# Performance work log

Hardware: AMD Instinct MI355X
Metric: run time of the kernel (lower is better)

The kernel has to match this reference:

```python
import jax, jax.numpy as jnp
import numpy as np

WIN = 32  # hardcoded window size in the original module


def _find(parent, x):
    while parent[x] != x:
        parent[x] = parent[parent[x]]
        x = parent[x]
    return x


def _label_background(bg):
    # 4-connected component labeling of True pixels; False pixels get label 0
    w = bg.shape[0]
    n = w * w
    parent = np.arange(n, dtype=np.int64)
    flat = bg.ravel()
    idx = np.arange(n).reshape(w, w)
    e1 = np.concatenate([idx[:, :-1].ravel(), idx[:-1, :].ravel()])
    e2 = np.concatenate([idx[:, 1:].ravel(), idx[1:, :].ravel()])
    for a, b in zip(e1, e2):
        if flat[a] and flat[b]:
            ra, rb = _find(parent, a), _find(parent, b)
            if ra != rb:
                parent[ra] = rb
    labels = np.zeros(n, dtype=np.int64)
    root2lab = {}
    nxt = 1
    for i in range(n):
        if flat[i]:
            r = _find(parent, i)
            if r not in root2lab:
                root2lab[r] = nxt
                nxt += 1
            labels[i] = root2lab[r]
    return labels


def _malis(seg, e1, e2, costs, pos):
    # Kruskal-style maximin MALIS edge weighting (descending affinity order).
    # Pairs involving segment label 0 (foreground / non-background) are excluded.
    n = seg.shape[0]
    parent = np.arange(n, dtype=np.int64)
    cnts = [({int(seg[i]): 1} if seg[i] != 0 else {}) for i in range(n)]
    w = np.zeros(costs.shape[0], dtype=np.int64)
    order = np.argsort(-costs, kind='stable')
    for e in order:
        a, b = _find(parent, e1[e]), _find(parent, e2[e])
        if a == b:
            continue
        ca, cb = cnts[a], cnts[b]
        if len(ca) > len(cb):  # small-to-large merge
            a, b, ca, cb = b, a, cb, ca
        common = 0
        for l, c in ca.items():
            if l in cb:
                common += c * cb[l]
        if pos:
            w[e] = common
        else:
            sa = sum(ca.values())
            sb = sum(cb.values())
            w[e] = sa * sb - common
        for l, c in ca.items():
            cb[l] = cb.get(l, 0) + c
        parent[a] = b
        cnts[a] = {}
    return w


def _malis_weights_full(pred, target):
    pred = np.asarray(pred)
    target = np.asarray(target)
    B, C, H, W = pred.shape
    weights_n = np.zeros(pred.shape, dtype=np.float32)
    weights_p = np.zeros(pred.shape, dtype=np.float32)
    idx = np.arange(WIN * WIN).reshape(WIN, WIN)
    e1 = np.concatenate([idx[:, :-1].ravel(), idx[:-1, :].ravel()])
    e2 = np.concatenate([idx[:, 1:].ravel(), idx[1:, :].ravel()])
    for r in range(H // WIN):
        for c in range(W // WIN):
            p = pred[:, :, r * WIN:(r + 1) * WIN, c * WIN:(c + 1) * WIN]
            t = target[:, :, r * WIN:(r + 1) * WIN, c * WIN:(c + 1) * WIN]
            costs_h = (p[:, :, :, :-1] + p[:, :, :, 1:]).reshape(B, -1)
            costs_v = (p[:, :, :-1, :] + p[:, :, 1:, :]).reshape(B, -1)
            costs = np.concatenate([costs_h, costs_v], 1)
            gt_h = (t[:, :, :, :-1] + t[:, :, :, 1:]).reshape(B, -1)
            gt_v = (t[:, :, :-1, :] + t[:, :, 1:, :]).reshape(B, -1)
            gt = np.concatenate([gt_h, gt_v], 1)
            costs_n = costs.copy()
            costs_p = costs.copy()
            costs_n[gt > 20] = 20
            costs_p[gt < 10] = 0
            gt = np.minimum(gt, 20)
            for i in range(B):
                seg = _label_background(t[i, 0] == 0)
                wn = _malis(seg, e1, e2, costs_n[i].astype(np.float32), 0).astype(np.float64)
                wp = _malis(seg, e1, e2, costs_p[i].astype(np.float32), 1).astype(np.float64)
                if wn.sum() > 0:
                    wn = wn / wn.sum()
                if wp.sum() > 0:
                    wp = wp / wp.sum()
                wn[gt[i] >= 10] = 0
                wp[gt[i] < 20] = 0
                half = WIN * (WIN - 1)
                for wsrc, wdst in ((wn, weights_n), (wp, weights_p)):
                    wh = wsrc[:half].reshape(WIN, WIN - 1)
                    wv = wsrc[half:].reshape(WIN - 1, WIN)
                    nw = np.zeros((WIN, WIN), dtype=np.float64)
                    nw[:, :-1] += wh
                    nw[:, 1:] += wh
                    nw[:-1, :] += wv
                    nw[1:, :] += wv
                    wdst[i, 0, r * WIN:(r + 1) * WIN, c * WIN:(c + 1) * WIN] = nw
    return weights_n, weights_p


def setup_inputs() -> dict:
    key = jax.random.key(0)
    k1, k2 = jax.random.split(key)
    y_true = jax.random.randint(k1, (4, 1, 256, 256), 0, 2).astype(jnp.float32) * 20.0
    y_pred = jax.random.uniform(k2, (4, 1, 256, 256), dtype=jnp.float32) * 20.0
    return {"y_true": y_true, "y_pred": y_pred}


def reference(y_true, y_pred):
    malis_lr = 1.0
    malis_lr_pos = 1.0
    out_sd = (jax.ShapeDtypeStruct(y_pred.shape, jnp.float32),
              jax.ShapeDtypeStruct(y_pred.shape, jnp.float32))
    weights_n, weights_p = jax.pure_callback(
        _malis_weights_full, out_sd,
        jax.lax.stop_gradient(y_pred), jax.lax.stop_gradient(y_true))
    loss_n = y_pred ** 2
    loss_p = (20.0 - y_pred) ** 2
    return (malis_lr * loss_n * weights_n + malis_lr_pos * loss_p * weights_p).sum()
```

## Files before the change

kernel.cpp:

```cpp
#include <hip/hip_runtime.h>

#define NPIX   1024
#define NEH    992
#define NEDGE  1984
#define SORTN  2048
#define CHUNK  8
#define NMERGE 1023
#define NIL    0xFFFFu

__device__ __forceinline__ void edge_ab(int e, int& a, int& b) {
    if (e < NEH) { int y = e / 31; int x = e - y * 31; a = y * 32 + x; b = a + 1; }
    else         { int ev = e - NEH; a = ev; b = ev + 32; }
}

__device__ __forceinline__ uint4 add4(uint4 x, uint4 y) {
    return make_uint4(x.x + y.x, x.y + y.y, x.z + y.z, x.w + y.w);
}
__device__ __forceinline__ uint4 sub4(uint4 x, uint4 y) {
    return make_uint4(x.x - y.x, x.y - y.y, x.z - y.z, x.w - y.w);
}

__device__ __forceinline__ unsigned rdl32(unsigned v, int lane) {
    return (unsigned)__builtin_amdgcn_readlane((int)v, lane);
}
__device__ __forceinline__ unsigned long long rdl64(unsigned long long v, int lane) {
    unsigned lo = (unsigned)__builtin_amdgcn_readlane((int)(unsigned)v, lane);
    unsigned hi = (unsigned)__builtin_amdgcn_readlane((int)(unsigned)(v >> 32), lane);
    return ((unsigned long long)hi << 32) | lo;
}

__device__ void ccl_body(char* smem, int* kprimeSh,
                         const float* __restrict__ t_glob,
                         unsigned short* __restrict__ pixLab_g,
                         int* __restrict__ Kg, int tileId) {
    const int tid = threadIdx.x;
    const int bat = tileId >> 6;
    const int tile = tileId & 63;
    const int tr = tile >> 3, tc = tile & 7;

    unsigned short* labS = (unsigned short*)smem;
    unsigned int*   cntS = (unsigned int*)(smem + 2048);
    unsigned char*  bgS  = (unsigned char*)(smem + 20480);

    for (int i = tid; i < NPIX; i += 256) {
        int y = i >> 5, x = i & 31;
        int gidx = bat * 65536 + (tr * 32 + y) * 256 + (tc * 32 + x);
        bgS[i] = (t_glob[gidx] == 0.0f) ? 1 : 0;
    }
    __syncthreads();

    if (tid < 64) {
        const int lane = tid;
        if (lane < 32) {
            #pragma unroll
            for (int x = 0; x < 32; x++) {
                int i = lane * 32 + x;
                labS[i] = bgS[i] ? (unsigned short)i : (unsigned short)NIL;
            }
        }
        while (true) {
            bool changed = false;
            if (lane < 32) {
                const int base = lane * 32;
                unsigned short v[32];
                #pragma unroll
                for (int x = 0; x < 32; x++) v[x] = labS[base + x];
                unsigned run = NIL;
                #pragma unroll
                for (int x = 0; x < 32; x++) {
                    unsigned val = v[x];
                    if (val == NIL) { run = NIL; }
                    else { unsigned nv = min(run, val); changed |= (nv != val); v[x] = (unsigned short)nv; run = nv; }
                }
                run = NIL;
                #pragma unroll
                for (int x = 31; x >= 0; x--) {
                    unsigned val = v[x];
                    if (val == NIL) { run = NIL; }
                    else { unsigned nv = min(run, val); changed |= (nv != val); v[x] = (unsigned short)nv; run = nv; }
                }
                #pragma unroll
                for (int x = 0; x < 32; x++) labS[base + x] = v[x];
            }
            if (lane < 32) {
                unsigned short c[32];
                #pragma unroll
                for (int k = 0; k < 32; k++) c[k] = labS[k * 32 + lane];
                unsigned run = NIL;
                #pragma unroll
                for (int k = 0; k < 32; k++) {
                    unsigned val = c[k];
                    if (val == NIL) { run = NIL; }
                    else { unsigned nv = min(run, val); changed |= (nv != val); c[k] = (unsigned short)nv; run = nv; }
                }
                run = NIL;
                #pragma unroll
                for (int k = 31; k >= 0; k--) {
                    unsigned val = c[k];
                    if (val == NIL) { run = NIL; }
                    else { unsigned nv = min(run, val); changed |= (nv != val); c[k] = (unsigned short)nv; run = nv; }
                }
                #pragma unroll
                for (int k = 0; k < 32; k++) labS[k * 32 + lane] = c[k];
            }
            if (!__any(changed)) break;
        }
    }
    __syncthreads();

    for (int i = tid; i < NPIX; i += 256) cntS[i] = 0;
    if (tid == 0) *kprimeSh = 0;
    __syncthreads();
    for (int i = tid; i < NPIX; i += 256)
        if (bgS[i]) atomicAdd(&cntS[labS[i]], 1u);
    __syncthreads();
    for (int i = tid; i < NPIX; i += 256) {
        if (bgS[i] && (int)labS[i] == i) {
            unsigned id = (cntS[i] >= 2) ? (unsigned)atomicAdd(kprimeSh, 1) : NIL;
            cntS[i] = id;
        }
    }
    __syncthreads();
    for (int i = tid; i < NPIX; i += 256)
        pixLab_g[tileId * NPIX + i] = bgS[i] ? (unsigned short)cntS[labS[i]] : (unsigned short)NIL;
    if (tid == 0) Kg[tileId] = *kprimeSh;
}

__device__ void sort_body(char* smem,
                          const float* __restrict__ t_glob,
                          const float* __restrict__ p_glob,
                          unsigned short* __restrict__ ord_g, int wg) {
    const int tid = threadIdx.x;
    const int sgn = wg & 1;
    const int tileId = wg >> 1;
    const int bat = tileId >> 6;
    const int tile = tileId & 63;
    const int tr = tile >> 3, tc = tile & 7;

    float*              pT   = (float*)smem;
    unsigned long long* keys = (unsigned long long*)(smem + 4096);
    unsigned char*      bgS  = (unsigned char*)(smem + 20480);

    for (int i = tid; i < NPIX; i += 256) {
        int y = i >> 5, x = i & 31;
        int gidx = bat * 65536 + (tr * 32 + y) * 256 + (tc * 32 + x);
        pT[i] = p_glob[gidx];
        bgS[i] = (t_glob[gidx] == 0.0f) ? 1 : 0;
    }
    __syncthreads();

    for (int k = tid; k < SORTN; k += 256) {
        unsigned long long key = 0ULL;
        if (k < NEDGE) {
            int a, b; edge_ab(k, a, b);
            float cost = pT[a] + pT[b];
            int nfg = (int)(!bgS[a]) + (int)(!bgS[b]);
            if (sgn == 0) { if (nfg == 2) cost = 20.0f; }
            else          { if (nfg == 0) cost = 0.0f;  }
            key = ((unsigned long long)__float_as_uint(cost) << 16)
                | (unsigned long long)(0xFFFFu - (unsigned)k);
        }
        keys[k] = key;
    }
    __syncthreads();
    for (int kk = 2; kk <= SORTN; kk <<= 1) {
        for (int jj = kk >> 1; jj > 0; jj >>= 1) {
            for (int i = tid; i < SORTN; i += 256) {
                int ixj = i ^ jj;
                if (ixj > i) {
                    unsigned long long A = keys[i], Bv = keys[ixj];
                    bool descBlk = ((i & kk) == 0);
                    if ((A < Bv) == descBlk) { keys[i] = Bv; keys[ixj] = A; }
                }
            }
            __syncthreads();
        }
    }
    for (int k = tid; k < NEDGE; k += 256)
        ord_g[(size_t)wg * SORTN + k] = (unsigned short)(0xFFFFu - (unsigned)(keys[k] & 0xFFFFULL));
}

__global__ __launch_bounds__(256, 2)
void k12_ccl_sort(const float* __restrict__ t_glob,
                  const float* __restrict__ p_glob,
                  unsigned short* __restrict__ pixLab_g,
                  int* __restrict__ Kg,
                  unsigned short* __restrict__ ord_g,
                  int nT) {
    __shared__ __align__(16) char smem[21504];
    __shared__ int kprimeSh;
    if ((int)blockIdx.x < nT)
        ccl_body(smem, &kprimeSh, t_glob, pixLab_g, Kg, blockIdx.x);
    else
        sort_body(smem, t_glob, p_glob, ord_g, blockIdx.x - nT);
}

__global__ __launch_bounds__(256, 2)
void k34_fused(const float* __restrict__ t_glob,
               const float* __restrict__ p_glob,
               const unsigned short* __restrict__ pixLab_g,
               const int* __restrict__ Kg,
               const unsigned short* __restrict__ ord_g,
               float* __restrict__ out) {
    const int tid = threadIdx.x;
    const int wg  = blockIdx.x;
    const int sgn = wg & 1;
    const int tileId = wg >> 1;
    const int bat = tileId >> 6;
    const int tile = tileId & 63;
    const int tr = tile >> 3, tc = tile & 7;

    __shared__ unsigned short parentS[NPIX];
    __shared__ unsigned long long nodeS[NPIX];
    __shared__ unsigned short nextS[NPIX];
    __shared__ unsigned int   mRecA[NMERGE];
    __shared__ unsigned int   mRecB[NMERGE];
    __shared__ unsigned int   mSaSb[NMERGE];
    __shared__ unsigned int   commonW[NMERGE];
    __shared__ unsigned short mEd[NMERGE];
    __shared__ float          pT[NPIX];
    __shared__ unsigned char  bgS[NPIX];
    __shared__ unsigned short pixLab[NPIX];
    __shared__ unsigned short posS[NPIX];
    __shared__ unsigned int   claimS[NPIX];
    __shared__ __align__(16) unsigned long long big[2564];
    __shared__ int   mCountSh;
    __shared__ unsigned wsumSh;
    __shared__ float lossSh;

    const unsigned short* ord = ord_g + (size_t)wg * SORTN;

    for (int i = tid; i < NPIX; i += 256) {
        int y = i >> 5, x = i & 31;
        int gidx = bat * 65536 + (tr * 32 + y) * 256 + (tc * 32 + x);
        float tv = t_glob[gidx];
        unsigned bg = (tv == 0.0f) ? 1u : 0u;
        pT[i] = p_glob[gidx];
        bgS[i] = (unsigned char)bg;
        pixLab[i] = pixLab_g[tileId * NPIX + i];
        parentS[i] = (unsigned short)i;
        nodeS[i] = ((unsigned long long)i << 48) | ((unsigned long long)i << 32)
                 | (1ULL << 16) | (unsigned long long)bg;
        nextS[i] = (unsigned short)NIL;
        claimS[i] = 0xFFFFFFFFu;
    }
    __syncthreads();

    if (tid < 64) {
        const int lane = tid;
        int m = 0;
        unsigned gen = 1u << 24;
        for (int kb = 0; kb < NEDGE; kb += 64) {
            int e = ord[kb + lane];
            int a, b; edge_ab(e, a, b);
            unsigned ra = (unsigned)a, rb = (unsigned)b;
            while (true) {
                unsigned pa = parentS[ra];
                unsigned pb = parentS[rb];
                if (pa == ra && pb == rb) break;
                if (pa != ra) { unsigned ga = parentS[pa]; parentS[ra] = (unsigned short)ga; ra = ga; }
                if (pb != rb) { unsigned gb = parentS[pb]; parentS[rb] = (unsigned short)gb; rb = gb; }
            }
            bool pending = (ra != rb);
            bool committed = false;
            unsigned recA = 0, recB = 0, recSS = 0;

            int winners = 64;
            while (__any(pending) && winners >= 6) {
                gen--;
                unsigned myval = (gen << 6) | (unsigned)lane;
                if (pending) {
                    atomicMin(&claimS[ra], myval);
                    atomicMin(&claimS[rb], myval);
                }
                bool win = pending && (claimS[ra] == myval) && (claimS[rb] == myval);
                if (win) {
                    unsigned long long nA = nodeS[ra], nB = nodeS[rb];
                    unsigned cons = ra, surv = rb;
                    unsigned szAu = (unsigned)(nA >> 16) & 0xFFFFu;
                    unsigned szBu = (unsigned)(nB >> 16) & 0xFFFFu;
                    if (szAu > szBu) {
                        unsigned t = cons; cons = surv; surv = t;
                        unsigned long long tn = nA; nA = nB; nB = tn;
                    }
                    unsigned headA = (unsigned)(nA >> 48);
                    unsigned tailA = (unsigned)(nA >> 32) & 0xFFFFu;
                    unsigned szA   = (unsigned)(nA >> 16) & 0xFFFFu;
                    unsigned slA   = (unsigned)nA & 0xFFFFu;
                    unsigned headB = (unsigned)(nB >> 48);
                    unsigned tailB = (unsigned)(nB >> 32) & 0xFFFFu;
                    unsigned szB   = (unsigned)(nB >> 16) & 0xFFFFu;
                    unsigned slB   = (unsigned)nB & 0xFFFFu;
                    unsigned long long merged =
                          ((unsigned long long)headA << 48)
                        | ((unsigned long long)tailB << 32)
                        | ((unsigned long long)(szA + szB) << 16)
                        | (unsigned long long)(slA + slB);
                    parentS[cons] = (unsigned short)surv;
                    nodeS[surv]   = merged;
                    nextS[tailA]  = (unsigned short)headB;
                    recA = (headA << 16) | headB;
                    recB = (szA << 16) | szB;
                    recSS = slA * slB;
                    committed = true;
                    pending = false;
                }
                winners = (int)__popcll(__ballot(win));
                if (pending) {
                    while (true) {
                        unsigned pa = parentS[ra];
                        unsigned pb = parentS[rb];
                        if (pa == ra && pb == rb) break;
                        if (pa != ra) { unsigned ga = parentS[pa]; parentS[ra] = (unsigned short)ga; ra = ga; }
                        if (pb != rb) { unsigned gb = parentS[pb]; parentS[rb] = (unsigned short)gb; rb = gb; }
                    }
                    if (ra == rb) pending = false;
                }
            }

            unsigned long long cmB = __ballot(committed);
            if (committed) {
                int idx = m + (int)__popcll(cmB & ((1ULL << lane) - 1ULL));
                mRecA[idx] = recA;
                mRecB[idx] = recB;
                mSaSb[idx] = recSS;
                mEd[idx]   = (unsigned short)e;
            }
            m += (int)__popcll(cmB);

            int logCount = 0;
            unsigned long long candm0 = __ballot(pending);
            if (candm0 != 0ULL) {
                unsigned long long na = 0, nb = 0;
                if (pending) { na = nodeS[ra]; nb = nodeS[rb]; }
                int j0 = __ffsll((long long)candm0) - 1;
                unsigned Ra = rdl32(ra, j0), Rb = rdl32(rb, j0);
                unsigned long long mAc = __ballot(pending && (ra == Ra || rb == Ra));
                unsigned long long mBc = __ballot(pending && (ra == Rb || rb == Rb));
                unsigned R = (__popcll(mAc) >= __popcll(mBc)) ? Ra : Rb;
                bool onR  = pending && ((ra == R) != (rb == R));
                bool offR = pending && (ra != R) && (rb != R);

                if (!__any(offR)) {
                    unsigned cons = 0;
                    unsigned long long cnode = 0;
                    if (onR) { cons = (ra == R) ? rb : ra; cnode = (ra == R) ? nb : na; }
                    gen--;
                    unsigned myval = (gen << 6) | (unsigned)lane;
                    if (onR) atomicMin(&claimS[cons], myval);
                    bool valid = onR && (claimS[cons] == myval);
                    unsigned long long vm = __ballot(valid);
                    if (vm != 0ULL) {
                        unsigned long long rnode = (R == Ra) ? rdl64(na, j0) : rdl64(nb, j0);
                        unsigned headR0 = (unsigned)(rnode >> 48);
                        unsigned tailR0 = (unsigned)(rnode >> 32) & 0xFFFFu;
                        unsigned szR0   = (unsigned)(rnode >> 16) & 0xFFFFu;
                        unsigned slR0   = (unsigned)rnode & 0xFFFFu;
                        unsigned headA = valid ? (unsigned)(cnode >> 48) : 0u;
                        unsigned tailA = valid ? (unsigned)(cnode >> 32) & 0xFFFFu : 0u;
                        unsigned szA   = valid ? (unsigned)(cnode >> 16) & 0xFFFFu : 0u;
                        unsigned slA   = valid ? (unsigned)cnode & 0xFFFFu : 0u;
                        unsigned s1 = szA, s2 = slA;
                        #pragma unroll
                        for (int d = 1; d < 64; d <<= 1) {
                            unsigned o1 = __shfl_up(s1, d, 64);
                            unsigned o2 = __shfl_up(s2, d, 64);
                            if (lane >= d) { s1 += o1; s2 += o2; }
                        }
                        unsigned szPre = s1 - szA, slPre = s2 - slA;
                        unsigned long long below = vm & ((1ULL << lane) - 1ULL);
                        int pv = 63 - (int)__clzll((long long)(below | 1ULL));
                        unsigned hprev = __shfl(headA, below ? pv : 0, 64);
                        unsigned headB = below ? hprev : headR0;
                        unsigned szB = szR0 + szPre;
                        unsigned slB = slR0 + slPre;
                        if (valid) {
                            parentS[cons] = (unsigned short)R;
                            nextS[tailA]  = (unsigned short)headB;
                            int idx = m + (int)__popcll(below);
                            mRecA[idx] = (headA << 16) | headB;
                            mRecB[idx] = (szA << 16) | szB;
                            mSaSb[idx] = slA * slB;
                            mEd[idx]   = (unsigned short)e;
                        }
                        int last = 63 - (int)__clzll((long long)vm);
                        if (valid && lane == last) {
                            nodeS[R] = ((unsigned long long)headA << 48)
                                     | ((unsigned long long)tailR0 << 32)
                                     | ((unsigned long long)(szR0 + s1) << 16)
                                     | (unsigned long long)(slR0 + s2);
                        }
                        logCount = (int)__popcll(vm);
                    }
                } else {
                    unsigned specAB = (ra << 16) | rb;
                    unsigned long long candm = candm0;
                    unsigned logRa  = 0xFFFFFFFFu;
                    unsigned logRbO = 0xFFFFFFFFu;
                    unsigned curRoot = 0xFFFFFFFFu;
                    unsigned long long logNode = 0;
                    while (candm != 0ULL) {
                        int j = __ffsll((long long)candm) - 1;
                        candm &= candm - 1ULL;
                        unsigned sAB = rdl32(specAB, j);
                        unsigned cra = sAB >> 16;
                        unsigned crb = sAB & 0xFFFFu;
                        unsigned long long hitA = __ballot(logRa == cra);
                        unsigned long long hitB = __ballot(logRa == crb);
                        if (hitA) cra = rdl32(curRoot, __ffsll((long long)hitA) - 1);
                        if (hitB) crb = rdl32(curRoot, __ffsll((long long)hitB) - 1);
                        if (cra == crb) continue;
                        unsigned ce = rdl32((unsigned)e, j);
                        unsigned long long hbA = __ballot(logRbO == cra);
                        unsigned long long hbB = __ballot(logRbO == crb);
                        unsigned long long cna = hbA ? rdl64(logNode, 63 - __clzll((long long)hbA)) : rdl64(na, j);
                        unsigned long long cnb = hbB ? rdl64(logNode, 63 - __clzll((long long)hbB)) : rdl64(nb, j);
                        unsigned cons = cra, surv = crb;
                        unsigned szAq = (unsigned)(cna >> 16) & 0xFFFFu;
                        unsigned szBq = (unsigned)(cnb >> 16) & 0xFFFFu;
                        if (szAq > szBq) {
                            unsigned t = cons; cons = surv; surv = t;
                            unsigned long long tn = cna; cna = cnb; cnb = tn;
                        }
                        unsigned headA = (unsigned)(cna >> 48);
                        unsigned tailA = (unsigned)(cna >> 32) & 0xFFFFu;
                        unsigned szA   = (unsigned)(cna >> 16) & 0xFFFFu;
                        unsigned slA   = (unsigned)cna & 0xFFFFu;
                        unsigned headB = (unsigned)(cnb >> 48);
                        unsigned tailB = (unsigned)(cnb >> 32) & 0xFFFFu;
                        unsigned szB   = (unsigned)(cnb >> 16) & 0xFFFFu;
                        unsigned slB   = (unsigned)cnb & 0xFFFFu;
                        unsigned long long merged =
                              ((unsigned long long)headA << 48)
                            | ((unsigned long long)tailB << 32)
                            | ((unsigned long long)(szA + szB) << 16)
                            | (unsigned long long)(slA + slB);
                        if (curRoot == cons) curRoot = surv;
                        if (lane == logCount) {
                            logRa = cons; logRbO = surv; curRoot = surv; logNode = merged;
                            parentS[cons] = (unsigned short)surv;
                            nodeS[surv]   = merged;
                            nextS[tailA]  = (unsigned short)headB;
                            int idx = m + logCount;
                            mRecA[idx] = (headA << 16) | headB;
                            mRecB[idx] = (szA << 16) | szB;
                            mSaSb[idx] = slA * slB;
                            mEd[idx]   = (unsigned short)ce;
                        }
                        logCount++;
                    }
                }
            }
            m += logCount;
        }
        if (lane == 0) mCountSh = m;
    }
    __syncthreads();
    const int M = mCountSh;
    const int K = Kg[tileId];
    for (int j = tid; j < M; j += 256) commonW[j] = 0;

    unsigned short* n0 = (unsigned short*)big;
    unsigned short* n1 = n0 + 1024;
    unsigned short* d0 = n0 + 2048;
    unsigned short* d1 = n0 + 3072;
    for (int i = tid; i < NPIX; i += 256) { n0[i] = nextS[i]; d0[i] = 1; }
    __syncthreads();
    for (int s = 0; s < 10; s++) {
        unsigned short* sn = (s & 1) ? n1 : n0;
        unsigned short* sd = (s & 1) ? d1 : d0;
        unsigned short* dn = (s & 1) ? n0 : n1;
        unsigned short* dd = (s & 1) ? d0 : d1;
        for (int i = tid; i < NPIX; i += 256) {
            unsigned nx = sn[i];
            unsigned dv = sd[i];
            if (nx != NIL) { dv += sd[nx]; nx = sn[nx]; }
            dn[i] = (unsigned short)nx;
            dd[i] = (unsigned short)dv;
        }
        __syncthreads();
    }
    for (int i = tid; i < NPIX; i += 256)
        posS[i] = (unsigned short)(NPIX - (int)d0[i]);
    __syncthreads();

    unsigned*       P32 = (unsigned*)big;
    uint4*          P4  = (uint4*)big;
    unsigned*       scr = P32 + 4100;
    uint4*          S4  = (uint4*)scr;
    unsigned short* P16 = (unsigned short*)big;
    for (int base = 0; base < K; base += CHUNK) {
        for (int idx = tid; idx < 4100; idx += 256) P32[idx] = 0;
        __syncthreads();
        for (int i = tid; i < NPIX; i += 256) {
            unsigned l = pixLab[i];
            if (l != NIL && l >= (unsigned)base && l < (unsigned)(base + CHUNK))
                P16[(posS[i] + 1) * 8 + (l - base)] = 1;
        }
        __syncthreads();
        {
            int r0 = tid * 4 + 1;
            uint4 acc = P4[r0];
            for (int rr = r0 + 1; rr <= r0 + 3; rr++) { acc = add4(acc, P4[rr]); P4[rr] = acc; }
            S4[tid] = acc;
            __syncthreads();
            if (tid < 64) {
                uint4 s0 = S4[tid * 4], s1 = S4[tid * 4 + 1], s2 = S4[tid * 4 + 2], s3 = S4[tid * 4 + 3];
                uint4 t1 = add4(s0, s1), t2 = add4(t1, s2), t3 = add4(t2, s3);
                uint4 run = t3;
                #pragma unroll
                for (int d = 1; d < 64; d <<= 1) {
                    uint4 o;
                    o.x = __shfl_up(run.x, d, 64);
                    o.y = __shfl_up(run.y, d, 64);
                    o.z = __shfl_up(run.z, d, 64);
                    o.w = __shfl_up(run.w, d, 64);
                    if (tid >= d) run = add4(run, o);
                }
                uint4 off = sub4(run, t3);
                S4[tid * 4]     = add4(s0, off);
                S4[tid * 4 + 1] = add4(t1, off);
                S4[tid * 4 + 2] = add4(t2, off);
                S4[tid * 4 + 3] = add4(t3, off);
            }
            __syncthreads();
            if (tid > 0) {
                uint4 off = S4[tid - 1];
                for (int rr = r0; rr <= r0 + 3; rr++) P4[rr] = add4(P4[rr], off);
            }
        }
        __syncthreads();
        for (int j = tid; j < M; j += 256) {
            unsigned recA = mRecA[j], recB = mRecB[j];
            unsigned aS = posS[recA >> 16];
            unsigned bS = posS[recA & 0xFFFFu];
            uint4 da = sub4(P4[aS + (recB >> 16)], P4[aS]);
            uint4 db = sub4(P4[bS + (recB & 0xFFFFu)], P4[bS]);
            unsigned acc;
            acc  = (da.x & 0xFFFFu) * (db.x & 0xFFFFu) + (da.x >> 16) * (db.x >> 16);
            acc += (da.y & 0xFFFFu) * (db.y & 0xFFFFu) + (da.y >> 16) * (db.y >> 16);
            acc += (da.z & 0xFFFFu) * (db.z & 0xFFFFu) + (da.z >> 16) * (db.z >> 16);
            acc += (da.w & 0xFFFFu) * (db.w & 0xFFFFu) + (da.w >> 16) * (db.w >> 16);
            commonW[j] += acc;
        }
        __syncthreads();
    }

    if (tid == 0) { wsumSh = 0; lossSh = 0.0f; }
    __syncthreads();
    unsigned wloc = 0;
    for (int j = tid; j < M; j += 256)
        wloc += (sgn == 0) ? (mSaSb[j] - commonW[j]) : commonW[j];
    if (wloc) atomicAdd(&wsumSh, wloc);
    __syncthreads();
    const unsigned wsum = wsumSh;
    if (wsum > 0) {
        const double inv = 1.0 / (double)wsum;
        float lloc = 0.0f;
        for (int j = tid; j < M; j += 256) {
            unsigned w = (sgn == 0) ? (mSaSb[j] - commonW[j]) : commonW[j];
            if (!w) continue;
            int e = mEd[j];
            int a, b; edge_ab(e, a, b);
            int nfg = (int)(!bgS[a]) + (int)(!bgS[b]);
            bool keep = (sgn == 0) ? (nfg == 0) : (nfg >= 1);
            if (!keep) continue;
            float wn = (float)((double)w * inv);
            float fa, fb;
            if (sgn == 0) { fa = pT[a] * pT[a];            fb = pT[b] * pT[b]; }
            else { float da = 20.0f - pT[a], db = 20.0f - pT[b]; fa = da * da; fb = db * db; }
            lloc += wn * (fa + fb);
        }
        if (lloc != 0.0f) atomicAdd(&lossSh, lloc);
        __syncthreads();
        if (tid == 0 && lossSh != 0.0f) atomicAdd(out, lossSh);
    }
}

__global__ __launch_bounds__(256, 2)
void malis_mono(const float* __restrict__ t_glob,
                const float* __restrict__ p_glob,
                float* __restrict__ out) {
    const int tid  = threadIdx.x;
    const int wg   = blockIdx.x;
    const int sgn  = wg & 1;
    const int tileId = wg >> 1;
    const int bat  = tileId >> 6;
    const int tile = tileId & 63;
    const int tr = tile >> 3, tc = tile & 7;

    __shared__ float          pT[NPIX];
    __shared__ unsigned char  bgS[NPIX];
    __shared__ unsigned short pixLab[NPIX];
    __shared__ unsigned short parentS[NPIX];
    __shared__ unsigned short nextS[NPIX];
    __shared__ unsigned long long nodeS[NPIX];
    __shared__ unsigned int   claimS[NPIX];
    __shared__ unsigned short posS[NPIX];
    __shared__ unsigned short orderS[NEDGE];
    __shared__ unsigned int   mRecA[NMERGE];
    __shared__ unsigned int   mRecB[NMERGE];
    __shared__ unsigned short mEd[NMERGE];
    __shared__ unsigned int   mSaSb[NMERGE];
    __shared__ unsigned int   commonW[NMERGE];
    __shared__ __align__(16) unsigned long long big[2564];
    __shared__ int   kprimeSh, mCountSh;
    __shared__ unsigned wsumSh;
    __shared__ float lossSh;

    for (int i = tid; i < NPIX; i += 256) {
        int y = i >> 5, x = i & 31;
        int gidx = bat * 65536 + (tr * 32 + y) * 256 + (tc * 32 + x);
        pT[i] = p_glob[gidx];
        bgS[i] = (t_glob[gidx] == 0.0f) ? 1 : 0;
    }
    __syncthreads();

    unsigned short* labS = (unsigned short*)big;
    unsigned int*   cntS = (unsigned int*)(((char*)big) + 2048);
    if (tid < 64) {
        const int lane = tid;
        if (lane < 32) {
            #pragma unroll
            for (int x = 0; x < 32; x++) {
                int i = lane * 32 + x;
                labS[i] = bgS[i] ? (unsigned short)i : (unsigned short)NIL;
            }
        }
        while (true) {
            bool changed = false;
            if (lane < 32) {
                const int base = lane * 32;
                unsigned short v[32];
                #pragma unroll
                for (int x = 0; x < 32; x++) v[x] = labS[base + x];
                unsigned run = NIL;
                #pragma unroll
                for (int x = 0; x < 32; x++) {
                    unsigned val = v[x];
                    if (val == NIL) { run = NIL; }
                    else { unsigned nv = min(run, val); changed |= (nv != val); v[x] = (unsigned short)nv; run = nv; }
                }
                run = NIL;
                #pragma unroll
                for (int x = 31; x >= 0; x--) {
                    unsigned val = v[x];
                    if (val == NIL) { run = NIL; }
                    else { unsigned nv = min(run, val); changed |= (nv != val); v[x] = (unsigned short)nv; run = nv; }
                }
                #pragma unroll
                for (int x = 0; x < 32; x++) labS[base + x] = v[x];
            }
            if (lane < 32) {
                unsigned short c[32];
                #pragma unroll
                for (int k = 0; k < 32; k++) c[k] = labS[k * 32 + lane];
                unsigned run = NIL;
                #pragma unroll
                for (int k = 0; k < 32; k++) {
                    unsigned val = c[k];
                    if (val == NIL) { run = NIL; }
                    else { unsigned nv = min(run, val); changed |= (nv != val); c[k] = (unsigned short)nv; run = nv; }
                }
                run = NIL;
                #pragma unroll
                for (int k = 31; k >= 0; k--) {
                    unsigned val = c[k];
                    if (val == NIL) { run = NIL; }
                    else { unsigned nv = min(run, val); changed |= (nv != val); c[k] = (unsigned short)nv; run = nv; }
                }
                #pragma unroll
                for (int k = 0; k < 32; k++) labS[k * 32 + lane] = c[k];
            }
            if (!__any(changed)) break;
        }
    }
    __syncthreads();

    for (int i = tid; i < NPIX; i += 256) cntS[i] = 0;
    if (tid == 0) kprimeSh = 0;
    __syncthreads();
    for (int i = tid; i < NPIX; i += 256)
        if (bgS[i]) atomicAdd(&cntS[labS[i]], 1u);
    __syncthreads();
    for (int i = tid; i < NPIX; i += 256) {
        if (bgS[i] && (int)labS[i] == i) {
            unsigned id = (cntS[i] >= 2) ? (unsigned)atomicAdd(&kprimeSh, 1) : NIL;
            cntS[i] = id;
        }
    }
    __syncthreads();
    for (int i = tid; i < NPIX; i += 256)
        pixLab[i] = bgS[i] ? (unsigned short)cntS[labS[i]] : (unsigned short)NIL;
    __syncthreads();
    const int K = kprimeSh;

    unsigned long long* keys = big;
    for (int k = tid; k < SORTN; k += 256) {
        unsigned long long key = 0ULL;
        if (k < NEDGE) {
            int a, b; edge_ab(k, a, b);
            float cost = pT[a] + pT[b];
            int nfg = (int)(!bgS[a]) + (int)(!bgS[b]);
            if (sgn == 0) { if (nfg == 2) cost = 20.0f; }
            else          { if (nfg == 0) cost = 0.0f;  }
            key = ((unsigned long long)__float_as_uint(cost) << 16)
                | (unsigned long long)(0xFFFFu - (unsigned)k);
        }
        keys[k] = key;
    }
    __syncthreads();
    for (int kk = 2; kk <= SORTN; kk <<= 1) {
        for (int jj = kk >> 1; jj > 0; jj >>= 1) {
            for (int i = tid; i < SORTN; i += 256) {
                int ixj = i ^ jj;
                if (ixj > i) {
                    unsigned long long A = keys[i], Bv = keys[ixj];
                    bool descBlk = ((i & kk) == 0);
                    if ((A < Bv) == descBlk) { keys[i] = Bv; keys[ixj] = A; }
                }
            }
            __syncthreads();
        }
    }
    for (int k = tid; k < NEDGE; k += 256)
        orderS[k] = (unsigned short)(0xFFFFu - (unsigned)(keys[k] & 0xFFFFULL));
    for (int i = tid; i < NPIX; i += 256) {
        parentS[i] = (unsigned short)i;
        nodeS[i] = ((unsigned long long)i << 48) | ((unsigned long long)i << 32)
                 | (1ULL << 16) | (unsigned long long)bgS[i];
        nextS[i] = (unsigned short)NIL;
    }
    __syncthreads();

    if (tid < 64) {
        const int lane = tid;
        int m = 0;
        for (int kb = 0; kb < NEDGE; kb += 64) {
            int e = orderS[kb + lane];
            int a, b; edge_ab(e, a, b);
            unsigned ra = (unsigned)a, rb = (unsigned)b;
            bool pending = true;
            bool committed = false;
            unsigned recA = 0, recB = 0, recSS = 0;
            while (__any(pending)) {
                if (pending) {
                    while (true) {
                        unsigned pa = parentS[ra];
                        unsigned pb = parentS[rb];
                        if (pa == ra && pb == rb) break;
                        if (pa != ra) { unsigned ga = parentS[pa]; parentS[ra] = (unsigned short)ga; ra = ga; }
                        if (pb != rb) { unsigned gb = parentS[pb]; parentS[rb] = (unsigned short)gb; rb = gb; }
                    }
                    if (ra == rb) pending = false;
                }
                if (pending) {
                    claimS[ra] = 0xFFFFFFFFu;
                    claimS[rb] = 0xFFFFFFFFu;
                }
                if (pending) {
                    atomicMin(&claimS[ra], (unsigned)lane);
                    atomicMin(&claimS[rb], (unsigned)lane);
                }
                bool win = pending && (claimS[ra] == (unsigned)lane) && (claimS[rb] == (unsigned)lane);
                if (win) {
                    unsigned long long nA = nodeS[ra], nB = nodeS[rb];
                    unsigned cons = ra, surv = rb;
                    unsigned szAu = (unsigned)(nA >> 16) & 0xFFFFu;
                    unsigned szBu = (unsigned)(nB >> 16) & 0xFFFFu;
                    if (szAu > szBu) {
                        unsigned t = cons; cons = surv; surv = t;
                        unsigned long long tn = nA; nA = nB; nB = tn;
                    }
                    unsigned headA = (unsigned)(nA >> 48);
                    unsigned tailA = (unsigned)(nA >> 32) & 0xFFFFu;
                    unsigned szA   = (unsigned)(nA >> 16) & 0xFFFFu;
                    unsigned slA   = (unsigned)nA & 0xFFFFu;
                    unsigned headB = (unsigned)(nB >> 48);
                    unsigned tailB = (unsigned)(nB >> 32) & 0xFFFFu;
                    unsigned szB   = (unsigned)(nB >> 16) & 0xFFFFu;
                    unsigned slB   = (unsigned)nB & 0xFFFFu;
                    unsigned long long merged =
                          ((unsigned long long)headA << 48)
                        | ((unsigned long long)tailB << 32)
                        | ((unsigned long long)(szA + szB) << 16)
                        | (unsigned long long)(slA + slB);
                    parentS[cons] = (unsigned short)surv;
                    nodeS[surv]   = merged;
                    nextS[tailA]  = (unsigned short)headB;
                    recA = (headA << 16) | headB;
                    recB = (szA << 16) | szB;
                    recSS = slA * slB;
                    committed = true;
                    pending = false;
                }
            }
            unsigned long long cm = __ballot(committed);
            if (committed) {
                int idx = m + (int)__popcll(cm & ((1ULL << lane) - 1ULL));
                mRecA[idx] = recA;
                mRecB[idx] = recB;
                mSaSb[idx] = recSS;
                mEd[idx]   = (unsigned short)e;
            }
            m += (int)__popcll(cm);
        }
        if (lane == 0) mCountSh = m;
    }
    __syncthreads();
    const int M = mCountSh;
    for (int j = tid; j < M; j += 256) commonW[j] = 0;

    unsigned short* n0 = (unsigned short*)big;
    unsigned short* n1 = n0 + 1024;
    unsigned short* d0 = n0 + 2048;
    unsigned short* d1 = n0 + 3072;
    for (int i = tid; i < NPIX; i += 256) { n0[i] = nextS[i]; d0[i] = 1; }
    __syncthreads();
    for (int s = 0; s < 10; s++) {
        unsigned short* sn = (s & 1) ? n1 : n0;
        unsigned short* sd = (s & 1) ? d1 : d0;
        unsigned short* dn = (s & 1) ? n0 : n1;
        unsigned short* dd = (s & 1) ? d0 : d1;
        for (int i = tid; i < NPIX; i += 256) {
            unsigned nx = sn[i];
            unsigned dv = sd[i];
            if (nx != NIL) { dv += sd[nx]; nx = sn[nx]; }
            dn[i] = (unsigned short)nx;
            dd[i] = (unsigned short)dv;
        }
        __syncthreads();
    }
    for (int i = tid; i < NPIX; i += 256)
        posS[i] = (unsigned short)(NPIX - (int)d0[i]);
    __syncthreads();

    unsigned*       P32 = (unsigned*)big;
    uint4*          P4  = (uint4*)big;
    unsigned*       scr = P32 + 4100;
    uint4*          S4  = (uint4*)scr;
    unsigned short* P16 = (unsigned short*)big;
    for (int base = 0; base < K; base += CHUNK) {
        for (int idx = tid; idx < 4100; idx += 256) P32[idx] = 0;
        __syncthreads();
        for (int i = tid; i < NPIX; i += 256) {
            unsigned l = pixLab[i];
            if (l != NIL && l >= (unsigned)base && l < (unsigned)(base + CHUNK))
                P16[(posS[i] + 1) * 8 + (l - base)] = 1;
        }
        __syncthreads();
        {
            int r0 = tid * 4 + 1;
            uint4 acc = P4[r0];
            for (int rr = r0 + 1; rr <= r0 + 3; rr++) { acc = add4(acc, P4[rr]); P4[rr] = acc; }
            S4[tid] = acc;
            __syncthreads();
            if (tid < 64) {
                uint4 s0 = S4[tid * 4], s1 = S4[tid * 4 + 1], s2 = S4[tid * 4 + 2], s3 = S4[tid * 4 + 3];
                uint4 t1 = add4(s0, s1), t2 = add4(t1, s2), t3 = add4(t2, s3);
                uint4 run = t3;
                #pragma unroll
                for (int d = 1; d < 64; d <<= 1) {
                    uint4 o;
                    o.x = __shfl_up(run.x, d, 64);
                    o.y = __shfl_up(run.y, d, 64);
                    o.z = __shfl_up(run.z, d, 64);
                    o.w = __shfl_up(run.w, d, 64);
                    if (tid >= d) run = add4(run, o);
                }
                uint4 off = sub4(run, t3);
                S4[tid * 4]     = add4(s0, off);
                S4[tid * 4 + 1] = add4(t1, off);
                S4[tid * 4 + 2] = add4(t2, off);
                S4[tid * 4 + 3] = add4(t3, off);
            }
            __syncthreads();
            if (tid > 0) {
                uint4 off = S4[tid - 1];
                for (int rr = r0; rr <= r0 + 3; rr++) P4[rr] = add4(P4[rr], off);
            }
        }
        __syncthreads();
        for (int j = tid; j < M; j += 256) {
            unsigned recA = mRecA[j], recB = mRecB[j];
            unsigned aS = posS[recA >> 16];
            unsigned bS = posS[recA & 0xFFFFu];
            uint4 da = sub4(P4[aS + (recB >> 16)], P4[aS]);
            uint4 db = sub4(P4[bS + (recB & 0xFFFFu)], P4[bS]);
            unsigned acc;
            acc  = (da.x & 0xFFFFu) * (db.x & 0xFFFFu) + (da.x >> 16) * (db.x >> 16);
            acc += (da.y & 0xFFFFu) * (db.y & 0xFFFFu) + (da.y >> 16) * (db.y >> 16);
            acc += (da.z & 0xFFFFu) * (db.z & 0xFFFFu) + (da.z >> 16) * (db.z >> 16);
            acc += (da.w & 0xFFFFu) * (db.w & 0xFFFFu) + (da.w >> 16) * (db.w >> 16);
            commonW[j] += acc;
        }
        __syncthreads();
    }

    if (tid == 0) { wsumSh = 0; lossSh = 0.0f; }
    __syncthreads();
    unsigned wloc = 0;
    for (int j = tid; j < M; j += 256)
        wloc += (sgn == 0) ? (mSaSb[j] - commonW[j]) : commonW[j];
    if (wloc) atomicAdd(&wsumSh, wloc);
    __syncthreads();
    const unsigned wsum = wsumSh;
    if (wsum > 0) {
        const double inv = 1.0 / (double)wsum;
        float lloc = 0.0f;
        for (int j = tid; j < M; j += 256) {
            unsigned w = (sgn == 0) ? (mSaSb[j] - commonW[j]) : commonW[j];
            if (!w) continue;
            int e = mEd[j];
            int a, b; edge_ab(e, a, b);
            int nfg = (int)(!bgS[a]) + (int)(!bgS[b]);
            bool keep = (sgn == 0) ? (nfg == 0) : (nfg >= 1);
            if (!keep) continue;
            float wn = (float)((double)w * inv);
            float fa, fb;
            if (sgn == 0) { fa = pT[a] * pT[a];            fb = pT[b] * pT[b]; }
            else { float da = 20.0f - pT[a], db = 20.0f - pT[b]; fa = da * da; fb = db * db; }
            lloc += wn * (fa + fb);
        }
        if (lloc != 0.0f) atomicAdd(&lossSh, lloc);
        __syncthreads();
        if (tid == 0 && lossSh != 0.0f) atomicAdd(out, lossSh);
    }
}

extern "C" void kernel_launch(void* const* d_in, const int* in_sizes, int n_in,
                              void* d_out, int out_size, void* d_ws, size_t ws_size,
                              hipStream_t stream) {
    const float* y_true = (const float*)d_in[0];
    const float* y_pred = (const float*)d_in[1];
    float* out = (float*)d_out;
    const int B  = in_sizes[0] / (256 * 256);
    const int nT = B * 64;
    const int nW = nT * 2;

    const size_t offK   = (size_t)nT * 2048;
    const size_t offOrd = offK + (((size_t)nT * 4 + 255) & ~(size_t)255);
    const size_t need   = offOrd + (size_t)nW * 4096;

    hipMemsetAsync(d_out, 0, (size_t)out_size * sizeof(float), stream);

    if (ws_size >= need) {
        char* ws = (char*)d_ws;
        unsigned short* pixLab_g = (unsigned short*)ws;
        int*            Kg       = (int*)(ws + offK);
        unsigned short* ord_g    = (unsigned short*)(ws + offOrd);
        hipLaunchKernelGGL(k12_ccl_sort, dim3(nT + nW), dim3(256), 0, stream,
                           y_true, y_pred, pixLab_g, Kg, ord_g, nT);
        hipLaunchKernelGGL(k34_fused,    dim3(nW), dim3(256), 0, stream,
                           y_true, y_pred, pixLab_g, Kg, ord_g, out);
    } else {
        hipLaunchKernelGGL(malis_mono, dim3(nW), dim3(256), 0, stream, y_true, y_pred, out);
    }
}
```

Measured before the change: 270.8 us.

## Finish low-parallelism union rounds with a serial wave-uniform merge tail

The parallel Kruskal merge loop now stops its claim/retry rounds once fewer than six lanes win in a round. The remaining pending edges are processed serially in edge order using wave-level broadcasts, with a register log of recent merges used to resolve roots without re-reading shared memory. Generation-tagged claim values remove the per-round reset of the claim array, and the initial root finding is hoisted out of the retry loop. The aim is to avoid long tails of nearly serial rounds, each paying atomics and barriers. The cost is more complex bookkeeping that must preserve exact merge order.

```diff
diff --git a/kernel.cpp b/kernel.cpp
--- a/kernel.cpp
+++ b/kernel.cpp
@@ -730,39 +730,37 @@
         nodeS[i] = ((unsigned long long)i << 48) | ((unsigned long long)i << 32)
                  | (1ULL << 16) | (unsigned long long)bgS[i];
         nextS[i] = (unsigned short)NIL;
+        claimS[i] = 0xFFFFFFFFu;
     }
     __syncthreads();
 
     if (tid < 64) {
         const int lane = tid;
         int m = 0;
+        unsigned gen = 1u << 24;
         for (int kb = 0; kb < NEDGE; kb += 64) {
             int e = orderS[kb + lane];
             int a, b; edge_ab(e, a, b);
             unsigned ra = (unsigned)a, rb = (unsigned)b;
-            bool pending = true;
+            while (true) {
+                unsigned pa = parentS[ra];
+                unsigned pb = parentS[rb];
+                if (pa == ra && pb == rb) break;
+                if (pa != ra) { unsigned ga = parentS[pa]; parentS[ra] = (unsigned short)ga; ra = ga; }
+                if (pb != rb) { unsigned gb = parentS[pb]; parentS[rb] = (unsigned short)gb; rb = gb; }
+            }
+            bool pending = (ra != rb);
             bool committed = false;
             unsigned recA = 0, recB = 0, recSS = 0;
-            while (__any(pending)) {
+            int winners = 64;
+            while (__any(pending) && winners >= 6) {
+                gen--;
+                unsigned myval = (gen << 6) | (unsigned)lane;
                 if (pending) {
-                    while (true) {
-                        unsigned pa = parentS[ra];
-                        unsigned pb = parentS[rb];
-                        if (pa == ra && pb == rb) break;
-                        if (pa != ra) { unsigned ga = parentS[pa]; parentS[ra] = (unsigned short)ga; ra = ga; }
-                        if (pb != rb) { unsigned gb = parentS[pb]; parentS[rb] = (unsigned short)gb; rb = gb; }
-                    }
-                    if (ra == rb) pending = false;
-                }
-                if (pending) {
-                    claimS[ra] = 0xFFFFFFFFu;
-                    claimS[rb] = 0xFFFFFFFFu;
-                }
-                if (pending) {
-                    atomicMin(&claimS[ra], (unsigned)lane);
-                    atomicMin(&claimS[rb], (unsigned)lane);
-                }
-                bool win = pending && (claimS[ra] == (unsigned)lane) && (claimS[rb] == (unsigned)lane);
+                    atomicMin(&claimS[ra], myval);
+                    atomicMin(&claimS[rb], myval);
+                }
+                bool win = pending && (claimS[ra] == myval) && (claimS[rb] == myval);
                 if (win) {
                     unsigned long long nA = nodeS[ra], nB = nodeS[rb];
                     unsigned cons = ra, surv = rb;
@@ -794,16 +792,91 @@
                     committed = true;
                     pending = false;
                 }
-            }
-            unsigned long long cm = __ballot(committed);
+                winners = (int)__popcll(__ballot(win));
+                if (pending) {
+                    while (true) {
+                        unsigned pa = parentS[ra];
+                        unsigned pb = parentS[rb];
+                        if (pa == ra && pb == rb) break;
+                        if (pa != ra) { unsigned ga = parentS[pa]; parentS[ra] = (unsigned short)ga; ra = ga; }
+                        if (pb != rb) { unsigned gb = parentS[pb]; parentS[rb] = (unsigned short)gb; rb = gb; }
+                    }
+                    if (ra == rb) pending = false;
+                }
+            }
+            unsigned long long cmB = __ballot(committed);
             if (committed) {
-                int idx = m + (int)__popcll(cm & ((1ULL << lane) - 1ULL));
+                int idx = m + (int)__popcll(cmB & ((1ULL << lane) - 1ULL));
                 mRecA[idx] = recA;
                 mRecB[idx] = recB;
                 mSaSb[idx] = recSS;
                 mEd[idx]   = (unsigned short)e;
             }
-            m += (int)__popcll(cm);
+            m += (int)__popcll(cmB);
+
+            int logCount = 0;
+            unsigned long long candm0 = __ballot(pending);
+            if (candm0 != 0ULL) {
+                unsigned long long na = 0, nb = 0;
+                if (pending) { na = nodeS[ra]; nb = nodeS[rb]; }
+                unsigned specAB = (ra << 16) | rb;
+                unsigned long long candm = candm0;
+                unsigned logRa  = 0xFFFFFFFFu;
+                unsigned logRbO = 0xFFFFFFFFu;
+                unsigned curRoot = 0xFFFFFFFFu;
+                unsigned long long logNode = 0;
+                while (candm != 0ULL) {
+                    int j = __ffsll((long long)candm) - 1;
+                    candm &= candm - 1ULL;
+                    unsigned sAB = rdl32(specAB, j);
+                    unsigned cra = sAB >> 16;
+                    unsigned crb = sAB & 0xFFFFu;
+                    unsigned long long hitA = __ballot(logRa == cra);
+                    unsigned long long hitB = __ballot(logRa == crb);
+                    if (hitA) cra = rdl32(curRoot, __ffsll((long long)hitA) - 1);
+                    if (hitB) crb = rdl32(curRoot, __ffsll((long long)hitB) - 1);
+                    if (cra == crb) continue;
+                    unsigned ce = rdl32((unsigned)e, j);
+                    unsigned long long hbA = __ballot(logRbO == cra);
+                    unsigned long long hbB = __ballot(logRbO == crb);
+                    unsigned long long cna = hbA ? rdl64(logNode, 63 - __clzll((long long)hbA)) : rdl64(na, j);
+                    unsigned long long cnb = hbB ? rdl64(logNode, 63 - __clzll((long long)hbB)) : rdl64(nb, j);
+                    unsigned cons = cra, surv = crb;
+                    unsigned szAq = (unsigned)(cna >> 16) & 0xFFFFu;
+                    unsigned szBq = (unsigned)(cnb >> 16) & 0xFFFFu;
+                    if (szAq > szBq) {
+                        unsigned t = cons; cons = surv; surv = t;
+                        unsigned long long tn = cna; cna = cnb; cnb = tn;
+                    }
+                    unsigned headA = (unsigned)(cna >> 48);
+                    unsigned tailA = (unsigned)(cna >> 32) & 0xFFFFu;
+                    unsigned szA   = (unsigned)(cna >> 16) & 0xFFFFu;
+                    unsigned slA   = (unsigned)cna & 0xFFFFu;
+                    unsigned headB = (unsigned)(cnb >> 48);
+                    unsigned tailB = (unsigned)(cnb >> 32) & 0xFFFFu;
+                    unsigned szB   = (unsigned)(cnb >> 16) & 0xFFFFu;
+                    unsigned slB   = (unsigned)cnb & 0xFFFFu;
+                    unsigned long long merged =
+                          ((unsigned long long)headA << 48)
+                        | ((unsigned long long)tailB << 32)
+                        | ((unsigned long long)(szA + szB) << 16)
+                        | (unsigned long long)(slA + slB);
+                    if (curRoot == cons) curRoot = surv;
+                    if (lane == logCount) {
+                        logRa = cons; logRbO = surv; curRoot = surv; logNode = merged;
+                        parentS[cons] = (unsigned short)surv;
+                        nodeS[surv]   = merged;
+                        nextS[tailA]  = (unsigned short)headB;
+                        int idx = m + logCount;
+                        mRecA[idx] = (headA << 16) | headB;
+                        mRecB[idx] = (szA << 16) | szB;
+                        mSaSb[idx] = slA * slB;
+                        mEd[idx]   = (unsigned short)ce;
+                    }
+                    logCount++;
+                }
+            }
+            m += logCount;
         }
         if (lane == 0) mCountSh = m;
     }
```

Result: no change. 269.9 us (-0.3%).
